# Optimization experiments

Hardware: AMD Instinct MI355X
Metric: run time of the kernel (lower is better)

Reference implementation:

```python
import jax, jax.numpy as jnp
import numpy as np

B, L, D, H = 4, 2048, 256, 8
FF = 128  # ff_intermediary_depth hard-coded in module
EPS = 1e-5


def layer_norm(x, g, b):
    mu = jnp.mean(x, axis=-1, keepdims=True)
    var = jnp.mean(jnp.square(x - mu), axis=-1, keepdims=True)
    return (x - mu) * jax.lax.rsqrt(var + EPS) * g + b


def setup_inputs() -> dict:
    key = jax.random.key(0)
    ks = jax.random.split(key, 8)
    s = 1.0 / np.sqrt(D)
    return {
        "seq": jax.random.normal(ks[0], (B, L, D), dtype=jnp.float32),
        "Wq": jax.random.normal(ks[1], (D, D * H), dtype=jnp.float32) * s,
        "Wk": jax.random.normal(ks[2], (D, D * H), dtype=jnp.float32) * s,
        "Wv": jax.random.normal(ks[3], (D, D * H), dtype=jnp.float32) * s,
        "Wo": jax.random.normal(ks[4], (D * H, D), dtype=jnp.float32) * (1.0 / np.sqrt(D * H)),
        "ln1_g": jnp.ones((D,), jnp.float32),
        "ln1_b": jnp.zeros((D,), jnp.float32),
        "W1": jax.random.normal(ks[5], (D, FF), dtype=jnp.float32) * s,
        "b1": jnp.zeros((FF,), jnp.float32),
        "W2": jax.random.normal(ks[6], (FF, D), dtype=jnp.float32) * (1.0 / np.sqrt(FF)),
        "b2": jnp.zeros((D,), jnp.float32),
        "ln2_g": jnp.ones((D,), jnp.float32),
        "ln2_b": jnp.zeros((D,), jnp.float32),
    }


def reference(seq, Wq, Wk, Wv, Wo, ln1_g, ln1_b, W1, b1, W2, b2, ln2_g, ln2_b):
    b, l, d = seq.shape
    # per-head dim equals full depth d (module quirk)
    q = (seq @ Wq).reshape(b, l, H, d)
    k = (seq @ Wk).reshape(b, l, H, d)
    v = (seq @ Wv).reshape(b, l, H, d)
    scores = jnp.einsum('bqhd,bkhd->bhqk', q, k) / jnp.sqrt(jnp.float32(d))
    a = jax.nn.softmax(scores, axis=-1)
    heads = jnp.einsum('bhqk,bkhd->bqhd', a, v).reshape(b, l, H * d)
    att_out = heads @ Wo
    x = layer_norm(seq + att_out, ln1_g, ln1_b)
    ff = jax.nn.relu(x @ W1 + b1) @ W2 + b2
    return layer_norm(x + ff, ln2_g, ln2_b)
```

## Files before the change

kernel.cpp:

```cpp
#include <hip/hip_runtime.h>


typedef unsigned short u16;
typedef unsigned int   u32;
typedef __bf16 bf16x8 __attribute__((ext_vector_type(8)));
typedef __bf16 bf16x2 __attribute__((ext_vector_type(2)));
typedef float  f32x4  __attribute__((ext_vector_type(4)));

#define MFMA(a, b, c) __builtin_amdgcn_mfma_f32_16x16x32_bf16(a, b, c, 0, 0, 0)

#if __has_builtin(__builtin_amdgcn_exp2f)
#define EXP2(x) __builtin_amdgcn_exp2f(x)
#else
#define EXP2(x) exp2f(x)
#endif

#if __has_builtin(__builtin_amdgcn_permlane16_swap) && \
    __has_builtin(__builtin_amdgcn_permlane32_swap)
#define HAS_PERMSWAP 1
#else
#define HAS_PERMSWAP 0
#endif

#define CEXP 0.09016844f

__device__ __forceinline__ float b2f(u16 h) {
  return __uint_as_float(((u32)h) << 16);
}
__device__ __forceinline__ u16 f2b(float f) {
  u32 u = __float_as_uint(f);
  u += 0x7FFFu + ((u >> 16) & 1u);
  return (u16)(u >> 16);
}
__device__ __forceinline__ u32 pkbf(float lo, float hi) {
  bf16x2 v;
  v[0] = (__bf16)lo;
  v[1] = (__bf16)hi;
  return __builtin_bit_cast(u32, v);
}
__device__ __forceinline__ bf16x8 ldb8(const u16* p) { return *(const bf16x8*)p; }

typedef const __attribute__((address_space(1))) u32* gas1_t;
typedef __attribute__((address_space(3))) u32* las3_t;
__device__ __forceinline__ void gload_lds16(const u16* g, u16* lds_base) {
  __builtin_amdgcn_global_load_lds((gas1_t)(const void*)g,
                                   (las3_t)(void*)lds_base, 16, 0, 0);
}

__device__ __forceinline__ int detect_f32(const void* seq) {
  const u32* s = (const u32*)seq;
  int cnt = 0;
  #pragma unroll
  for (int i = 0; i < 64; i++) {
    u32 e = (s[i] >> 7) & 0xFFu;
    cnt += (e >= 100u && e <= 140u) ? 1 : 0;
  }
  return cnt < 48;
}

__device__ __forceinline__ u16 ldw(const void* W, size_t idx, int isf32) {
  return isf32 ? f2b(((const float*)W)[idx]) : ((const u16*)W)[idx];
}

#if HAS_PERMSWAP
__device__ __forceinline__ bf16x8 softmax_pa(f32x4 sn0, f32x4 sn1,
                                             float& lsum) {
  float p00 = EXP2(sn0[0]), p01 = EXP2(sn0[1]);
  float p02 = EXP2(sn0[2]), p03 = EXP2(sn0[3]);
  float p10 = EXP2(sn1[0]), p11 = EXP2(sn1[1]);
  float p12 = EXP2(sn1[2]), p13 = EXP2(sn1[3]);
  lsum += ((p00 + p01) + (p02 + p03)) + ((p10 + p11) + (p12 + p13));
  u32 A0 = pkbf(p00, p01), A1 = pkbf(p02, p03);
  u32 B0 = pkbf(p10, p11), B1 = pkbf(p12, p13);
  auto ra = __builtin_amdgcn_permlane32_swap(A0, B0, false, false);
  auto rb = __builtin_amdgcn_permlane32_swap(A1, B1, false, false);
  auto sa = __builtin_amdgcn_permlane16_swap(ra[0], ra[1], false, false);
  auto sb = __builtin_amdgcn_permlane16_swap(rb[0], rb[1], false, false);
  uint4 wv;
  wv.x = sa[0];
  wv.y = sb[0];
  wv.z = sa[1];
  wv.w = sb[1];
  return __builtin_bit_cast(bf16x8, wv);
}
#endif

__device__ __forceinline__ void ingest_body(
    int bx, int tid, int isf32,
    const void* __restrict__ seq, const void* __restrict__ g1,
    const void* __restrict__ be1, const void* __restrict__ b1,
    const void* __restrict__ b2v, const void* __restrict__ g2,
    const void* __restrict__ be2, u16* __restrict__ sbuf,
    u16* __restrict__ vecs) {
  if (bx < 2048) {
    size_t i = (size_t)bx * 1024 + tid * 4;
    if (isf32) {
      const float* sp = (const float*)seq;
      u16 o0 = f2b(sp[i]), o1 = f2b(sp[i + 1]), o2 = f2b(sp[i + 2]), o3 = f2b(sp[i + 3]);
      uint2 ov; ov.x = (u32)o0 | ((u32)o1 << 16); ov.y = (u32)o2 | ((u32)o3 << 16);
      *(uint2*)(sbuf + i) = ov;
    } else {
      *(uint2*)(sbuf + i) = ((const uint2*)seq)[i >> 2];
    }
  } else {
    int t = bx - 2048;
    const void* src; int n;
    switch (t) {
      case 0: src = g1;  n = 256; break;
      case 1: src = be1; n = 256; break;
      case 2: src = b1;  n = 128; break;
      case 3: src = b2v; n = 256; break;
      case 4: src = g2;  n = 256; break;
      default: src = be2; n = 256; break;
    }
    if (tid < n) vecs[t * 256 + tid] = ldw(src, tid, isf32);
  }
}

__device__ __forceinline__ void pack_body(
    int px, int py, int tid, int isf32,
    const void* __restrict__ Wq, const void* __restrict__ Wk,
    const void* __restrict__ Wv, const void* __restrict__ Wo,
    const void* __restrict__ W1, const void* __restrict__ W2,
    u16* __restrict__ pWq, u16* __restrict__ pWk, u16* __restrict__ pWv,
    u16* __restrict__ pWo, u16* __restrict__ pW1, u16* __restrict__ pW2) {
  const void* W; u16* P; int K, N;
  switch (py) {
    case 0: W = Wq; P = pWq; K = 256;  N = 2048; break;
    case 1: W = Wk; P = pWk; K = 256;  N = 2048; break;
    case 2: W = Wv; P = pWv; K = 256;  N = 2048; break;
    case 3: W = Wo; P = pWo; K = 2048; N = 256;  break;
    case 4: W = W1; P = pW1; K = 256;  N = 128;  break;
    default: W = W2; P = pW2; K = 128; N = 256;  break;
  }
  int t = px * 256 + tid;
  int total = (K >> 5) * (N >> 4) * 64;
  if (t >= total) return;
  int lane = t & 63, f = t >> 6;
  int NT = N >> 4;
  int kt = f / NT, nt = f - kt * NT;
  int row0 = kt * 32 + ((lane >> 4) << 3);
  int col = nt * 16 + (lane & 15);
  u16 e[8];
  #pragma unroll
  for (int j = 0; j < 8; j++) e[j] = ldw(W, (size_t)(row0 + j) * N + col, isf32);
  uint4 u;
  u.x = (u32)e[0] | ((u32)e[1] << 16);
  u.y = (u32)e[2] | ((u32)e[3] << 16);
  u.z = (u32)e[4] | ((u32)e[5] << 16);
  u.w = (u32)e[6] | ((u32)e[7] << 16);
  *(uint4*)(P + ((size_t)f * 64 + lane) * 8) = u;
}

__global__ __launch_bounds__(256) void ingest_pack_kernel(
    const void* __restrict__ seq, const void* __restrict__ g1,
    const void* __restrict__ be1, const void* __restrict__ b1,
    const void* __restrict__ b2v, const void* __restrict__ g2,
    const void* __restrict__ be2, u16* __restrict__ sbuf,
    u16* __restrict__ vecs,
    const void* __restrict__ Wq, const void* __restrict__ Wk,
    const void* __restrict__ Wv, const void* __restrict__ Wo,
    const void* __restrict__ W1, const void* __restrict__ W2,
    u16* __restrict__ pWq, u16* __restrict__ pWk, u16* __restrict__ pWv,
    u16* __restrict__ pWo, u16* __restrict__ pW1, u16* __restrict__ pW2) {
  int isf32 = detect_f32(seq);
  int bx = blockIdx.x, tid = threadIdx.x;
  if (bx < 2054) {
    ingest_body(bx, tid, isf32, seq, g1, be1, b1, b2v, g2, be2, sbuf, vecs);
  } else {
    int bxp = bx - 2054;
    pack_body(bxp & 255, bxp >> 8, tid, isf32, Wq, Wk, Wv, Wo, W1, W2,
              pWq, pWk, pWv, pWo, pW1, pW2);
  }
}

__global__ __launch_bounds__(256, 2) void qkv_kernel(
    const u16* __restrict__ X,
    const u16* __restrict__ pWq, const u16* __restrict__ pWk,
    const u16* __restrict__ pWv,
    u16* __restrict__ Qo, u16* __restrict__ Ko, u16* __restrict__ Vo,
    int ntbase, int hc) {
  __shared__ u16 blds[64 * 512];
  const u16* Pw = (blockIdx.z == 0) ? pWq : ((blockIdx.z == 1) ? pWk : pWv);
  u16* Out = (blockIdx.z == 0) ? Qo : ((blockIdx.z == 1) ? Ko : Vo);
  int tid = threadIdx.x, lane = tid & 63, w = tid >> 6;
  int nt0 = ntbase + blockIdx.x * 8;
  int m0 = blockIdx.y * 128 + w * 32;
  bf16x8 af[2][8];
  #pragma unroll
  for (int kt = 0; kt < 8; kt++) {
    af[0][kt] = ldb8(X + (size_t)(m0 + (lane & 15)) * 256 + kt * 32 + (lane >> 4) * 8);
    af[1][kt] = ldb8(X + (size_t)(m0 + 16 + (lane & 15)) * 256 + kt * 32 + (lane >> 4) * 8);
  }
  #pragma unroll
  for (int i = 0; i < 16; i++) {
    int fl = w + i * 4;
    int kt = fl >> 3, nt = fl & 7;
    gload_lds16(Pw + ((size_t)(kt * 128 + nt0 + nt) * 64 + lane) * 8,
                blds + (size_t)fl * 512);
  }
  asm volatile("s_waitcnt vmcnt(0)" ::: "memory");
  __syncthreads();
  f32x4 acc[2][8] = {};
  #pragma unroll
  for (int kt = 0; kt < 8; kt++) {
    const u16* bp = blds + (size_t)kt * 8 * 512 + (size_t)lane * 8;
    #pragma unroll
    for (int nt = 0; nt < 8; nt++) {
      bf16x8 b = ldb8(bp + nt * 512);
      acc[0][nt] = MFMA(af[0][kt], b, acc[0][nt]);
      acc[1][nt] = MFMA(af[1][kt], b, acc[1][nt]);
    }
  }
  int isv = (blockIdx.z == 2);
  float sc = (blockIdx.z == 0) ? CEXP : 1.0f;
  int hl = blockIdx.x >> 1;
  int dd0 = (blockIdx.x & 1) * 128;
  int m0b = blockIdx.y * 128;
  int bi = m0b >> 11, l0 = m0b & 2047;
  __syncthreads();
  if (!isv) {
    #pragma unroll
    for (int mt = 0; mt < 2; mt++)
      #pragma unroll
      for (int nt = 0; nt < 8; nt++)
        #pragma unroll
        for (int r = 0; r < 4; r++)
          blds[(w * 32 + mt * 16 + (lane >> 4) * 4 + r) * 136 + nt * 16 + (lane & 15)] =
              f2b(acc[mt][nt][r] * sc);
    __syncthreads();
    #pragma unroll
    for (int i = 0; i < 8; i++) {
      int c = tid + i * 256;
      int mloc = c >> 4, q = c & 15;
      uint4 v = *(uint4*)(blds + mloc * 136 + q * 8);
      *(uint4*)(Out + ((size_t)(bi * hc + hl) * 2048 + l0 + mloc) * 256 + dd0 + q * 8) = v;
    }
  } else {
    #pragma unroll
    for (int mt = 0; mt < 2; mt++)
      #pragma unroll
      for (int nt = 0; nt < 8; nt++)
        #pragma unroll
        for (int r = 0; r < 4; r++)
          blds[(nt * 16 + (lane & 15)) * 136 + w * 32 + mt * 16 + (lane >> 4) * 4 + r] =
              f2b(acc[mt][nt][r]);
    __syncthreads();
    #pragma unroll
    for (int i = 0; i < 8; i++) {
      int c = tid + i * 256;
      int nloc = c >> 4, q = c & 15;
      uint4 v = *(uint4*)(blds + nloc * 136 + q * 8);
      *(uint4*)(Out + ((size_t)(bi * hc + hl) * 256 + dd0 + nloc) * 2048 + l0 + q * 8) = v;
    }
  }
}

__global__ __launch_bounds__(512, 4) void attn_kernel(
    const u16* __restrict__ Q, const u16* __restrict__ K,
    const u16* __restrict__ Vt, u16* __restrict__ O, int nbh) {
  __shared__ u16 kbuf[2 * 8192];
  __shared__ u16 vbuf[2 * 8192];
#if !HAS_PERMSWAP
  __shared__ u16 plds[8 * 640];
#endif
  int tid = threadIdx.x, lane = tid & 63, w = tid >> 6;
  int bi2 = blockIdx.x;
  int bh, qt;
  if (nbh >= 8) {
    int G = nbh >> 3;
    bh = (bi2 & 7) * G + (bi2 >> 3) % G;
    qt = bi2 / (8 * G);
  } else {
    bh = bi2 % nbh; qt = bi2 / nbh;
  }
  const u16* Qb  = Q  + (size_t)bh * 2048 * 256;
  const u16* Kb  = K  + (size_t)bh * 2048 * 256;
  const u16* Vtb = Vt + (size_t)bh * 256 * 2048;
  u16* Ob = O + (size_t)bh * 2048 * 256;
  int q0 = qt * 128 + w * 16;
  bf16x8 qf[8];
  #pragma unroll
  for (int kt = 0; kt < 8; kt++)
    qf[kt] = ldb8(Qb + (size_t)(q0 + (lane & 15)) * 256 + kt * 32 + (lane >> 4) * 8);
  f32x4 o[16] = {};
  float lsum = 0.f;
#if !HAS_PERMSWAP
  u16* pl = plds + (size_t)w * 640;
#endif

  #pragma unroll
  for (int j = 0; j < 2; j++) {
    int f = w * 2 + j;
    gload_lds16(Kb + (size_t)((f >> 3) * 16 + (lane & 15)) * 256 +
                    (f & 7) * 32 + (lane >> 4) * 8,
                kbuf + f * 512);
    gload_lds16(Vtb + (size_t)(f * 16 + (lane & 15)) * 2048 + (lane >> 4) * 8,
                vbuf + f * 512);
  }

  for (int t = 0; t < 64; t++) {
    int s0i = t * 32;
    asm volatile("s_waitcnt vmcnt(0)\ns_barrier" ::: "memory");
    if (t < 63) {
      int nb = (t + 1) & 1;
      #pragma unroll
      for (int j = 0; j < 2; j++) {
        int f = w * 2 + j;
        gload_lds16(Kb + (size_t)(s0i + 32 + (f >> 3) * 16 + (lane & 15)) * 256 +
                        (f & 7) * 32 + (lane >> 4) * 8,
                    kbuf + nb * 8192 + f * 512);
        gload_lds16(Vtb + (size_t)(f * 16 + (lane & 15)) * 2048 + s0i + 32 +
                        (lane >> 4) * 8,
                    vbuf + nb * 8192 + f * 512);
      }
    }
    const u16* kb = kbuf + (t & 1) * 8192;
    f32x4 s[2] = {};
    __builtin_amdgcn_s_setprio(1);
    #pragma unroll
    for (int ntk = 0; ntk < 2; ntk++)
      #pragma unroll
      for (int kt = 0; kt < 8; kt++) {
        bf16x8 a = ldb8(kb + (size_t)(ntk * 8 + kt) * 512 + lane * 8);
        s[ntk] = MFMA(a, qf[kt], s[ntk]);
      }
    __builtin_amdgcn_s_setprio(0);
#if HAS_PERMSWAP
    bf16x8 pa = softmax_pa(s[0], s[1], lsum);
#else
    #pragma unroll
    for (int ntk = 0; ntk < 2; ntk++) {
      float p0 = EXP2(s[ntk][0]);
      float p1 = EXP2(s[ntk][1]);
      float p2 = EXP2(s[ntk][2]);
      float p3 = EXP2(s[ntk][3]);
      lsum += (p0 + p1) + (p2 + p3);
      uint2 pk;
      pk.x = pkbf(p0, p1);
      pk.y = pkbf(p2, p3);
      *(uint2*)(pl + (lane & 15) * 40 + 16 * ntk + 4 * (lane >> 4)) = pk;
    }
    asm volatile("s_waitcnt lgkmcnt(0)" ::: "memory");
    bf16x8 pa = ldb8(pl + (lane & 15) * 40 + (lane >> 4) * 8);
    asm volatile("s_waitcnt lgkmcnt(0)" ::: "memory");
#endif
    const u16* vb0 = vbuf + (t & 1) * 8192;
    __builtin_amdgcn_s_setprio(1);
    #pragma unroll
    for (int nt = 0; nt < 16; nt++) {
      bf16x8 vb = ldb8(vb0 + (size_t)nt * 512 + lane * 8);
      o[nt] = MFMA(vb, pa, o[nt]);
    }
    __builtin_amdgcn_s_setprio(0);
  }
  float l = lsum;
  l += __shfl_xor(l, 16);
  l += __shfl_xor(l, 32);
  float linv = 1.0f / l;
  u16* el = kbuf + w * 1152;
  __syncthreads();
  #pragma unroll
  for (int g = 0; g < 4; g++) {
    if (g) asm volatile("s_waitcnt lgkmcnt(0)" ::: "memory");
    #pragma unroll
    for (int t2 = 0; t2 < 4; t2++) {
      int nt = g * 4 + t2;
      uint2 pk;
      pk.x = pkbf(o[nt][0] * linv, o[nt][1] * linv);
      pk.y = pkbf(o[nt][2] * linv, o[nt][3] * linv);
      *(uint2*)(el + (lane & 15) * 72 + t2 * 16 + 4 * (lane >> 4)) = pk;
    }
    asm volatile("s_waitcnt lgkmcnt(0)" ::: "memory");
    #pragma unroll
    for (int rep = 0; rep < 2; rep++) {
      int ch = lane + rep * 64;
      int row = ch >> 3, c8 = ch & 7;
      uint4 v = *(uint4*)(el + row * 72 + c8 * 8);
      *(uint4*)(Ob + (size_t)(q0 + row) * 256 + g * 64 + c8 * 8) = v;
    }
  }
}

__global__ __launch_bounds__(128) void accum_ln1_ffn_ln2_kernel(
    const u16* __restrict__ Oc, const u16* __restrict__ pWo,
    const u16* __restrict__ sbuf, const u16* __restrict__ vecs,
    const u16* __restrict__ pW1, const u16* __restrict__ pW2,
    const void* __restrict__ seq, void* __restrict__ out) {
  __shared__ u16 blds[2 * 32 * 512];
  int tid = threadIdx.x, lane = tid & 63, w = tid >> 6;
  int m0 = blockIdx.x * 32 + w * 16;
  int arow = m0 + (lane & 15);
  int bq = arow >> 11, lrow = arow & 2047;
  f32x4 acc[16] = {};
  #pragma unroll
  for (int i = 0; i < 16; i++) {
    int fl = w + i * 2;
    int ktg = fl >> 4, nt = fl & 15;
    gload_lds16(pWo + ((size_t)(ktg * 16 + nt) * 64 + lane) * 8,
                blds + (size_t)fl * 512);
  }
  asm volatile("s_waitcnt vmcnt(0)" ::: "memory");
  __syncthreads();
  for (int r = 0; r < 32; r++) {
    int k0 = r * 2;
    const u16* cur = blds + (size_t)(r & 1) * 16384;
    bf16x8 aA, aB;
    {
      int ktl = k0, hl = ktl >> 3;
      int d0 = (ktl & 7) * 32 + (lane >> 4) * 8;
      aA = ldb8(Oc + ((size_t)(bq * 8 + hl) * 2048 + lrow) * 256 + d0);
      ktl = k0 + 1; hl = ktl >> 3;
      d0 = (ktl & 7) * 32 + (lane >> 4) * 8;
      aB = ldb8(Oc + ((size_t)(bq * 8 + hl) * 2048 + lrow) * 256 + d0);
    }
    if (r < 31) {
      u16* nxt = blds + (size_t)((r + 1) & 1) * 16384;
      #pragma unroll
      for (int i = 0; i < 16; i++) {
        int fl = w + i * 2;
        int ktg = k0 + 2 + (fl >> 4), nt = fl & 15;
        gload_lds16(pWo + ((size_t)(ktg * 16 + nt) * 64 + lane) * 8,
                    nxt + (size_t)fl * 512);
      }
    }
    #pragma unroll
    for (int kl = 0; kl < 2; kl++) {
      bf16x8 a = kl ? aB : aA;
      const u16* bp = cur + (size_t)kl * 16 * 512 + (size_t)lane * 8;
      #pragma unroll
      for (int nt = 0; nt < 16; nt++) {
        bf16x8 b = ldb8(bp + nt * 512);
        acc[nt] = MFMA(a, b, acc[nt]);
      }
    }
    asm volatile("s_waitcnt vmcnt(0)" ::: "memory");
    __syncthreads();
  }
  int rbase = m0 + (lane >> 4) * 4;
  #pragma unroll
  for (int nt = 0; nt < 16; nt++) {
    int d = nt * 16 + (lane & 15);
    #pragma unroll
    for (int r = 0; r < 4; r++)
      acc[nt][r] += b2f(sbuf[(size_t)(rbase + r) * 256 + d]);
  }
  float mu[4], rs[4];
  #pragma unroll
  for (int r = 0; r < 4; r++) {
    float sm = 0.f;
    #pragma unroll
    for (int nt = 0; nt < 16; nt++) sm += acc[nt][r];
    sm += __shfl_xor(sm, 1); sm += __shfl_xor(sm, 2);
    sm += __shfl_xor(sm, 4); sm += __shfl_xor(sm, 8);
    mu[r] = sm * (1.0f / 256.0f);
    float v = 0.f;
    #pragma unroll
    for (int nt = 0; nt < 16; nt++) { float dd = acc[nt][r] - mu[r]; v += dd * dd; }
    v += __shfl_xor(v, 1); v += __shfl_xor(v, 2);
    v += __shfl_xor(v, 4); v += __shfl_xor(v, 8);
    rs[r] = rsqrtf(v * (1.0f / 256.0f) + 1e-5f);
  }
  u16* xw = blds + (size_t)w * 16 * 264;
  uint2 xp[16];
  #pragma unroll
  for (int nt = 0; nt < 16; nt++) {
    int d = nt * 16 + (lane & 15);
    float gg = b2f(vecs[d]), bb = b2f(vecs[256 + d]);
    u16 e[4];
    #pragma unroll
    for (int r = 0; r < 4; r++) {
      e[r] = f2b((acc[nt][r] - mu[r]) * rs[r] * gg + bb);
      xw[((lane >> 4) * 4 + r) * 264 + d] = e[r];
    }
    xp[nt].x = (u32)e[0] | ((u32)e[1] << 16);
    xp[nt].y = (u32)e[2] | ((u32)e[3] << 16);
  }
  __syncthreads();
  int isf32 = detect_f32(seq);
  u16* hb = blds + 16384 + (size_t)w * 16 * 136;
  f32x4 acc1[8] = {};
  #pragma unroll
  for (int kt = 0; kt < 8; kt++) {
    bf16x8 a = ldb8(xw + (size_t)(lane & 15) * 264 + kt * 32 + (lane >> 4) * 8);
    const u16* bp = pW1 + ((size_t)kt * 8 * 64 + lane) * 8;
    #pragma unroll
    for (int nt = 0; nt < 8; nt++) {
      bf16x8 b = ldb8(bp + nt * 512);
      acc1[nt] = MFMA(a, b, acc1[nt]);
    }
  }
  #pragma unroll
  for (int nt = 0; nt < 8; nt++) {
    int col = nt * 16 + (lane & 15);
    float bb = b2f(vecs[512 + col]);
    #pragma unroll
    for (int r = 0; r < 4; r++) {
      float h = fmaxf(acc1[nt][r] + bb, 0.f);
      hb[((lane >> 4) * 4 + r) * 136 + col] = f2b(h);
    }
  }
  __syncthreads();
  f32x4 acc2[16] = {};
  #pragma unroll
  for (int ks = 0; ks < 4; ks++) {
    bf16x8 a = ldb8(hb + (size_t)(lane & 15) * 136 + ks * 32 + (lane >> 4) * 8);
    const u16* bp = pW2 + ((size_t)ks * 16 * 64 + lane) * 8;
    #pragma unroll
    for (int nt = 0; nt < 16; nt++) {
      bf16x8 b = ldb8(bp + nt * 512);
      acc2[nt] = MFMA(a, b, acc2[nt]);
    }
  }
  #pragma unroll
  for (int nt = 0; nt < 16; nt++) {
    int d = nt * 16 + (lane & 15);
    float bb = b2f(vecs[768 + d]);
    acc2[nt][0] += bb + b2f((u16)(xp[nt].x & 0xFFFF));
    acc2[nt][1] += bb + b2f((u16)(xp[nt].x >> 16));
    acc2[nt][2] += bb + b2f((u16)(xp[nt].y & 0xFFFF));
    acc2[nt][3] += bb + b2f((u16)(xp[nt].y >> 16));
  }
  float mu2[4], rs2[4];
  #pragma unroll
  for (int r = 0; r < 4; r++) {
    float sm = 0.f;
    #pragma unroll
    for (int nt = 0; nt < 16; nt++) sm += acc2[nt][r];
    sm += __shfl_xor(sm, 1); sm += __shfl_xor(sm, 2);
    sm += __shfl_xor(sm, 4); sm += __shfl_xor(sm, 8);
    mu2[r] = sm * (1.0f / 256.0f);
    float v = 0.f;
    #pragma unroll
    for (int nt = 0; nt < 16; nt++) { float dd = acc2[nt][r] - mu2[r]; v += dd * dd; }
    v += __shfl_xor(v, 1); v += __shfl_xor(v, 2);
    v += __shfl_xor(v, 4); v += __shfl_xor(v, 8);
    rs2[r] = rsqrtf(v * (1.0f / 256.0f) + 1e-5f);
  }
  #pragma unroll
  for (int nt = 0; nt < 16; nt++) {
    int d = nt * 16 + (lane & 15);
    float gg = b2f(vecs[1024 + d]), bb = b2f(vecs[1280 + d]);
    #pragma unroll
    for (int r = 0; r < 4; r++) {
      float val = (acc2[nt][r] - mu2[r]) * rs2[r] * gg + bb;
      size_t idx = (size_t)(rbase + r) * 256 + d;
      if (isf32) ((float*)out)[idx] = val;
      else       ((u16*)out)[idx]   = f2b(val);
    }
  }
}

__global__ __launch_bounds__(256) void accum_kernel(
    const u16* __restrict__ Oc, const u16* __restrict__ pWo,
    float* __restrict__ att_out, int kt0, int hc) {
  __shared__ u16 blds[64 * 512];
  int tid = threadIdx.x, lane = tid & 63, w = tid >> 6;
  int m0 = blockIdx.x * 64 + w * 16;
  int arow = m0 + (lane & 15);
  int bq = arow >> 11, lrow = arow & 2047;
  int ktn = hc * 8;
  f32x4 acc[16] = {};
  for (int k0 = 0; k0 < ktn; k0 += 4) {
    __syncthreads();
    #pragma unroll
    for (int i = 0; i < 16; i++) {
      int fl = w + i * 4;
      int ktg = kt0 + k0 + (fl >> 4), nt = fl & 15;
      gload_lds16(pWo + ((size_t)(ktg * 16 + nt) * 64 + lane) * 8,
                  blds + (size_t)fl * 512);
    }
    asm volatile("s_waitcnt vmcnt(0)" ::: "memory");
    __syncthreads();
    #pragma unroll
    for (int kl = 0; kl < 4; kl++) {
      int ktl = k0 + kl;
      int hl = ktl >> 3;
      int d0 = (ktl & 7) * 32 + (lane >> 4) * 8;
      bf16x8 a = ldb8(Oc + ((size_t)(bq * hc + hl) * 2048 + lrow) * 256 + d0);
      const u16* bp = blds + (size_t)kl * 16 * 512 + (size_t)lane * 8;
      #pragma unroll
      for (int nt = 0; nt < 16; nt++) {
        bf16x8 b = ldb8(bp + nt * 512);
        acc[nt] = MFMA(a, b, acc[nt]);
      }
    }
  }
  int rbase = m0 + (lane >> 4) * 4;
  #pragma unroll
  for (int nt = 0; nt < 16; nt++) {
    int d = nt * 16 + (lane & 15);
    #pragma unroll
    for (int r = 0; r < 4; r++)
      att_out[(size_t)(rbase + r) * 256 + d] += acc[nt][r];
  }
}

__global__ __launch_bounds__(256) void ln1_kernel(
    const float* __restrict__ att_out, const u16* __restrict__ sbuf,
    const u16* __restrict__ vecs, u16* __restrict__ xout) {
  int tid = threadIdx.x, lane = tid & 63, w = tid >> 6;
  int row = blockIdx.x * 4 + w;
  const float* ar = att_out + (size_t)row * 256;
  f32x4 a = *(const f32x4*)(ar + lane * 4);
  uint2 sv = *(const uint2*)(sbuf + (size_t)row * 256 + lane * 4);
  float y[4];
  y[0] = a[0] + b2f((u16)(sv.x & 0xFFFF));
  y[1] = a[1] + b2f((u16)(sv.x >> 16));
  y[2] = a[2] + b2f((u16)(sv.y & 0xFFFF));
  y[3] = a[3] + b2f((u16)(sv.y >> 16));
  float sm = y[0] + y[1] + y[2] + y[3];
  sm += __shfl_xor(sm, 1);  sm += __shfl_xor(sm, 2);  sm += __shfl_xor(sm, 4);
  sm += __shfl_xor(sm, 8);  sm += __shfl_xor(sm, 16); sm += __shfl_xor(sm, 32);
  float mu = sm * (1.0f / 256.0f);
  float v = 0.f;
  #pragma unroll
  for (int j = 0; j < 4; j++) { float d = y[j] - mu; v += d * d; }
  v += __shfl_xor(v, 1);  v += __shfl_xor(v, 2);  v += __shfl_xor(v, 4);
  v += __shfl_xor(v, 8);  v += __shfl_xor(v, 16); v += __shfl_xor(v, 32);
  float rs = rsqrtf(v * (1.0f / 256.0f) + 1e-5f);
  u16 o[4];
  #pragma unroll
  for (int j = 0; j < 4; j++) {
    int d = lane * 4 + j;
    o[j] = f2b((y[j] - mu) * rs * b2f(vecs[d]) + b2f(vecs[256 + d]));
  }
  uint2 ov; ov.x = (u32)o[0] | ((u32)o[1] << 16); ov.y = (u32)o[2] | ((u32)o[3] << 16);
  *(uint2*)(xout + (size_t)row * 256 + lane * 4) = ov;
}

__global__ __launch_bounds__(128) void ffn_ln2_kernel(
    const u16* __restrict__ x, const u16* __restrict__ pW1,
    const u16* __restrict__ pW2, const u16* __restrict__ vecs,
    const void* __restrict__ seq, void* __restrict__ out) {
  __shared__ u16 hbuf[2 * 16 * 136];
  int isf32 = detect_f32(seq);
  int tid = threadIdx.x, lane = tid & 63, w = tid >> 6;
  int m0 = blockIdx.x * 32 + w * 16;
  int arow = m0 + (lane & 15);
  u16* hb = hbuf + w * 16 * 136;
  f32x4 acc1[8] = {};
  #pragma unroll
  for (int kt = 0; kt < 8; kt++) {
    bf16x8 a = ldb8(x + (size_t)arow * 256 + kt * 32 + (lane >> 4) * 8);
    const u16* bp = pW1 + ((size_t)kt * 8 * 64 + lane) * 8;
    #pragma unroll
    for (int nt = 0; nt < 8; nt++) {
      bf16x8 b = ldb8(bp + nt * 512);
      acc1[nt] = MFMA(a, b, acc1[nt]);
    }
  }
  #pragma unroll
  for (int nt = 0; nt < 8; nt++) {
    int col = nt * 16 + (lane & 15);
    float bb = b2f(vecs[512 + col]);
    #pragma unroll
    for (int r = 0; r < 4; r++) {
      float h = fmaxf(acc1[nt][r] + bb, 0.f);
      hb[((lane >> 4) * 4 + r) * 136 + col] = f2b(h);
    }
  }
  __syncthreads();
  f32x4 acc2[16] = {};
  #pragma unroll
  for (int ks = 0; ks < 4; ks++) {
    bf16x8 a = ldb8(hb + (lane & 15) * 136 + ks * 32 + (lane >> 4) * 8);
    const u16* bp = pW2 + ((size_t)ks * 16 * 64 + lane) * 8;
    #pragma unroll
    for (int nt = 0; nt < 16; nt++) {
      bf16x8 b = ldb8(bp + nt * 512);
      acc2[nt] = MFMA(a, b, acc2[nt]);
    }
  }
  int rbase = m0 + (lane >> 4) * 4;
  #pragma unroll
  for (int nt = 0; nt < 16; nt++) {
    int d = nt * 16 + (lane & 15);
    float bb = b2f(vecs[768 + d]);
    #pragma unroll
    for (int r = 0; r < 4; r++)
      acc2[nt][r] += bb + b2f(x[(size_t)(rbase + r) * 256 + d]);
  }
  float mu[4], rs[4];
  #pragma unroll
  for (int r = 0; r < 4; r++) {
    float sm = 0.f;
    #pragma unroll
    for (int nt = 0; nt < 16; nt++) sm += acc2[nt][r];
    sm += __shfl_xor(sm, 1); sm += __shfl_xor(sm, 2);
    sm += __shfl_xor(sm, 4); sm += __shfl_xor(sm, 8);
    mu[r] = sm * (1.0f / 256.0f);
    float v = 0.f;
    #pragma unroll
    for (int nt = 0; nt < 16; nt++) { float dd = acc2[nt][r] - mu[r]; v += dd * dd; }
    v += __shfl_xor(v, 1); v += __shfl_xor(v, 2);
    v += __shfl_xor(v, 4); v += __shfl_xor(v, 8);
    rs[r] = rsqrtf(v * (1.0f / 256.0f) + 1e-5f);
  }
  #pragma unroll
  for (int nt = 0; nt < 16; nt++) {
    int d = nt * 16 + (lane & 15);
    float gg = b2f(vecs[1024 + d]), bb = b2f(vecs[1280 + d]);
    #pragma unroll
    for (int r = 0; r < 4; r++) {
      float val = (acc2[nt][r] - mu[r]) * rs[r] * gg + bb;
      size_t idx = (size_t)(rbase + r) * 256 + d;
      if (isf32) ((float*)out)[idx] = val;
      else       ((u16*)out)[idx]   = f2b(val);
    }
  }
}

__global__ __launch_bounds__(256) void sentinel_kernel(void* out, int n,
                                                       const void* seq) {
  int isf32 = detect_f32(seq);
  int i = blockIdx.x * 256 + threadIdx.x;
  if (i < n) {
    if (isf32) ((float*)out)[i] = 777.0f;
    else       ((u16*)out)[i]   = 0x4442;
  }
}

extern "C" void kernel_launch(void* const* d_in, const int* in_sizes, int n_in,
                              void* d_out, int out_size, void* d_ws, size_t ws_size,
                              hipStream_t stream) {
  (void)in_sizes; (void)n_in;
  const void* seq  = d_in[0];
  const void* Wq   = d_in[1];
  const void* Wk   = d_in[2];
  const void* Wv   = d_in[3];
  const void* Wo   = d_in[4];
  const void* g1   = d_in[5];
  const void* be1  = d_in[6];
  const void* W1   = d_in[7];
  const void* b1   = d_in[8];
  const void* W2   = d_in[9];
  const void* b2   = d_in[10];
  const void* g2   = d_in[11];
  const void* be2  = d_in[12];

  size_t o = 0;
  u16* ws = (u16*)d_ws;
  u16* pWq = ws + o; o += 524288;
  u16* pWk = ws + o; o += 524288;
  u16* pWv = ws + o; o += 524288;
  u16* pWo = ws + o; o += 524288;
  u16* pW1 = ws + o; o += 32768;
  u16* pW2 = ws + o; o += 32768;
  float* att = (float*)(ws + o); o += 4194304;
  u16* xb   = ws + o; o += 2097152;
  u16* sbuf = ws + o; o += 2097152;
  u16* vecs = ws + o; o += 2048;
  size_t fixed_elems = o;

  int hc = 0;
  for (int c = 8; c >= 1; c >>= 1) {
    size_t need = (fixed_elems + (size_t)4 * c * 2097152) * 2;
    if (need <= ws_size) { hc = c; break; }
  }
  if (hc == 0) {
    sentinel_kernel<<<dim3((out_size + 255) / 256), 256, 0, stream>>>(
        d_out, out_size, seq);
    return;
  }
  u16* Qc = ws + o; o += (size_t)hc * 2097152;
  u16* Kc = ws + o; o += (size_t)hc * 2097152;
  u16* Vc = ws + o; o += (size_t)hc * 2097152;
  u16* Oc = ws + o;

  ingest_pack_kernel<<<dim3(2054 + 1536), 256, 0, stream>>>(
      seq, g1, be1, b1, b2, g2, be2, sbuf, vecs,
      Wq, Wk, Wv, Wo, W1, W2, pWq, pWk, pWv, pWo, pW1, pW2);
  if (hc == 8) {
    qkv_kernel<<<dim3(16, 64, 3), 256, 0, stream>>>(
        sbuf, pWq, pWk, pWv, Qc, Kc, Vc, 0, 8);
    attn_kernel<<<dim3(32 * 16), 512, 0, stream>>>(Qc, Kc, Vc, Oc, 32);
    accum_ln1_ffn_ln2_kernel<<<dim3(256), 128, 0, stream>>>(
        Oc, pWo, sbuf, vecs, pW1, pW2, seq, (void*)d_out);
  } else {
    hipMemsetAsync(att, 0, 2097152 * sizeof(float), stream);
    int nchunks = 8 / hc;
    for (int c = 0; c < nchunks; c++) {
      int nbh = 4 * hc;
      qkv_kernel<<<dim3(2 * hc, 64, 3), 256, 0, stream>>>(
          sbuf, pWq, pWk, pWv, Qc, Kc, Vc, c * hc * 16, hc);
      attn_kernel<<<dim3(nbh * 16), 512, 0, stream>>>(Qc, Kc, Vc, Oc, nbh);
      accum_kernel<<<dim3(128), 256, 0, stream>>>(Oc, pWo, att, c * hc * 8, hc);
    }
    ln1_kernel<<<dim3(2048), 256, 0, stream>>>(att, sbuf, vecs, xb);
    ffn_ln2_kernel<<<dim3(256), 128, 0, stream>>>(xb, pW1, pW2, vecs, seq,
                                                  (void*)d_out);
  }
}
```

Baseline: 341.8 us.

## Reuse staged QKV weight tile across four row blocks per workgroup

Each qkv workgroup now handles 512 rows instead of 128, looping four times over the same weight tile held in LDS, so weight loads into LDS are cut by a factor of four. The activation fragments for the next row block are prefetched while the current one is being computed. The epilogue now stages through a small per-wave LDS buffer instead of the block-wide buffer, which removes block-level barriers. The grid shrinks fourfold (768 blocks), which may reduce occupancy and latency hiding, and the extra LDS buffer raises LDS use per block.

```diff
diff --git a/kernel.cpp b/kernel.cpp
--- a/kernel.cpp
+++ b/kernel.cpp
@@ -181,17 +181,16 @@
     u16* __restrict__ Qo, u16* __restrict__ Ko, u16* __restrict__ Vo,
     int ntbase, int hc) {
   __shared__ u16 blds[64 * 512];
+  __shared__ u16 ebuf[4 * 1280];
   const u16* Pw = (blockIdx.z == 0) ? pWq : ((blockIdx.z == 1) ? pWk : pWv);
   u16* Out = (blockIdx.z == 0) ? Qo : ((blockIdx.z == 1) ? Ko : Vo);
   int tid = threadIdx.x, lane = tid & 63, w = tid >> 6;
   int nt0 = ntbase + blockIdx.x * 8;
-  int m0 = blockIdx.y * 128 + w * 32;
-  bf16x8 af[2][8];
-  #pragma unroll
-  for (int kt = 0; kt < 8; kt++) {
-    af[0][kt] = ldb8(X + (size_t)(m0 + (lane & 15)) * 256 + kt * 32 + (lane >> 4) * 8);
-    af[1][kt] = ldb8(X + (size_t)(m0 + 16 + (lane & 15)) * 256 + kt * 32 + (lane >> 4) * 8);
-  }
+  int isv = (blockIdx.z == 2);
+  float sc = (blockIdx.z == 0) ? CEXP : 1.0f;
+  int hl = blockIdx.x >> 1;
+  int dd0 = (blockIdx.x & 1) * 128;
+  u16* eb = ebuf + (size_t)w * 1280;
   #pragma unroll
   for (int i = 0; i < 16; i++) {
     int fl = w + i * 4;
@@ -199,59 +198,87 @@
     gload_lds16(Pw + ((size_t)(kt * 128 + nt0 + nt) * 64 + lane) * 8,
                 blds + (size_t)fl * 512);
   }
+  bf16x8 af[2][8];
+  {
+    int m0 = blockIdx.y * 512 + w * 32;
+    #pragma unroll
+    for (int kt = 0; kt < 8; kt++) {
+      af[0][kt] = ldb8(X + (size_t)(m0 + (lane & 15)) * 256 + kt * 32 + (lane >> 4) * 8);
+      af[1][kt] = ldb8(X + (size_t)(m0 + 16 + (lane & 15)) * 256 + kt * 32 + (lane >> 4) * 8);
+    }
+  }
   asm volatile("s_waitcnt vmcnt(0)" ::: "memory");
   __syncthreads();
-  f32x4 acc[2][8] = {};
-  #pragma unroll
-  for (int kt = 0; kt < 8; kt++) {
-    const u16* bp = blds + (size_t)kt * 8 * 512 + (size_t)lane * 8;
-    #pragma unroll
-    for (int nt = 0; nt < 8; nt++) {
-      bf16x8 b = ldb8(bp + nt * 512);
-      acc[0][nt] = MFMA(af[0][kt], b, acc[0][nt]);
-      acc[1][nt] = MFMA(af[1][kt], b, acc[1][nt]);
-    }
-  }
-  int isv = (blockIdx.z == 2);
-  float sc = (blockIdx.z == 0) ? CEXP : 1.0f;
-  int hl = blockIdx.x >> 1;
-  int dd0 = (blockIdx.x & 1) * 128;
-  int m0b = blockIdx.y * 128;
-  int bi = m0b >> 11, l0 = m0b & 2047;
-  __syncthreads();
-  if (!isv) {
-    #pragma unroll
-    for (int mt = 0; mt < 2; mt++)
+  for (int y = 0; y < 4; y++) {
+    int m0b = blockIdx.y * 512 + y * 128;
+    f32x4 acc[2][8] = {};
+    #pragma unroll
+    for (int kt = 0; kt < 8; kt++) {
+      const u16* bp = blds + (size_t)kt * 8 * 512 + (size_t)lane * 8;
       #pragma unroll
-      for (int nt = 0; nt < 8; nt++)
+      for (int nt = 0; nt < 8; nt++) {
+        bf16x8 b = ldb8(bp + nt * 512);
+        acc[0][nt] = MFMA(af[0][kt], b, acc[0][nt]);
+        acc[1][nt] = MFMA(af[1][kt], b, acc[1][nt]);
+      }
+    }
+    if (y < 3) {
+      int m1 = m0b + 128 + w * 32;
+      #pragma unroll
+      for (int kt = 0; kt < 8; kt++) {
+        af[0][kt] = ldb8(X + (size_t)(m1 + (lane & 15)) * 256 + kt * 32 + (lane >> 4) * 8);
+        af[1][kt] = ldb8(X + (size_t)(m1 + 16 + (lane & 15)) * 256 + kt * 32 + (lane >> 4) * 8);
+      }
+    }
+    int bi = m0b >> 11, l0 = m0b & 2047;
+    if (!isv) {
+      #pragma unroll
+      for (int g = 0; g < 4; g++) {
         #pragma unroll
-        for (int r = 0; r < 4; r++)
-          blds[(w * 32 + mt * 16 + (lane >> 4) * 4 + r) * 136 + nt * 16 + (lane & 15)] =
-              f2b(acc[mt][nt][r] * sc);
-    __syncthreads();
-    #pragma unroll
-    for (int i = 0; i < 8; i++) {
-      int c = tid + i * 256;
-      int mloc = c >> 4, q = c & 15;
-      uint4 v = *(uint4*)(blds + mloc * 136 + q * 8);
-      *(uint4*)(Out + ((size_t)(bi * hc + hl) * 2048 + l0 + mloc) * 256 + dd0 + q * 8) = v;
-    }
-  } else {
-    #pragma unroll
-    for (int mt = 0; mt < 2; mt++)
+        for (int mt = 0; mt < 2; mt++)
+          #pragma unroll
+          for (int nt2 = 0; nt2 < 2; nt2++) {
+            int nt = g * 2 + nt2;
+            #pragma unroll
+            for (int r = 0; r < 4; r++)
+              eb[(mt * 16 + (lane >> 4) * 4 + r) * 40 + nt2 * 16 + (lane & 15)] =
+                  f2b(acc[mt][nt][r] * sc);
+          }
+        asm volatile("s_waitcnt lgkmcnt(0)" ::: "memory");
+        #pragma unroll
+        for (int rep = 0; rep < 2; rep++) {
+          int ch = lane + rep * 64;
+          int row = ch >> 2, c8 = ch & 3;
+          uint4 v = *(uint4*)(eb + row * 40 + c8 * 8);
+          *(uint4*)(Out + ((size_t)(bi * hc + hl) * 2048 + l0 + w * 32 + row) * 256 +
+                    dd0 + g * 32 + c8 * 8) = v;
+        }
+        asm volatile("s_waitcnt lgkmcnt(0)" ::: "memory");
+      }
+    } else {
       #pragma unroll
-      for (int nt = 0; nt < 8; nt++)
+      for (int g = 0; g < 4; g++) {
         #pragma unroll
-        for (int r = 0; r < 4; r++)
-          blds[(nt * 16 + (lane & 15)) * 136 + w * 32 + mt * 16 + (lane >> 4) * 4 + r] =
-              f2b(acc[mt][nt][r]);
-    __syncthreads();
-    #pragma unroll
-    for (int i = 0; i < 8; i++) {
-      int c = tid + i * 256;
-      int nloc = c >> 4, q = c & 15;
-      uint4 v = *(uint4*)(blds + nloc * 136 + q * 8);
-      *(uint4*)(Out + ((size_t)(bi * hc + hl) * 256 + dd0 + nloc) * 2048 + l0 + q * 8) = v;
+        for (int mt = 0; mt < 2; mt++)
+          #pragma unroll
+          for (int nt2 = 0; nt2 < 2; nt2++) {
+            int nt = g * 2 + nt2;
+            #pragma unroll
+            for (int r = 0; r < 4; r++)
+              eb[(nt2 * 16 + (lane & 15)) * 40 + mt * 16 + (lane >> 4) * 4 + r] =
+                  f2b(acc[mt][nt][r]);
+          }
+        asm volatile("s_waitcnt lgkmcnt(0)" ::: "memory");
+        #pragma unroll
+        for (int rep = 0; rep < 2; rep++) {
+          int ch = lane + rep * 64;
+          int dc = ch >> 2, c8 = ch & 3;
+          uint4 v = *(uint4*)(eb + dc * 40 + c8 * 8);
+          *(uint4*)(Out + ((size_t)(bi * hc + hl) * 256 + dd0 + g * 32 + dc) * 2048 +
+                    l0 + w * 32 + c8 * 8) = v;
+        }
+        asm volatile("s_waitcnt lgkmcnt(0)" ::: "memory");
+      }
     }
   }
 }
@@ -772,7 +799,7 @@
       seq, g1, be1, b1, b2, g2, be2, sbuf, vecs,
       Wq, Wk, Wv, Wo, W1, W2, pWq, pWk, pWv, pWo, pW1, pW2);
   if (hc == 8) {
-    qkv_kernel<<<dim3(16, 64, 3), 256, 0, stream>>>(
+    qkv_kernel<<<dim3(16, 16, 3), 256, 0, stream>>>(
         sbuf, pWq, pWk, pWv, Qc, Kc, Vc, 0, 8);
     attn_kernel<<<dim3(32 * 16), 512, 0, stream>>>(Qc, Kc, Vc, Oc, 32);
     accum_ln1_ffn_ln2_kernel<<<dim3(256), 128, 0, stream>>>(
@@ -782,7 +809,7 @@
     int nchunks = 8 / hc;
     for (int c = 0; c < nchunks; c++) {
       int nbh = 4 * hc;
-      qkv_kernel<<<dim3(2 * hc, 64, 3), 256, 0, stream>>>(
+      qkv_kernel<<<dim3(2 * hc, 16, 3), 256, 0, stream>>>(
           sbuf, pWq, pWk, pWv, Qc, Kc, Vc, c * hc * 16, hc);
       attn_kernel<<<dim3(nbh * 16), 512, 0, stream>>>(Qc, Kc, Vc, Oc, nbh);
       accum_kernel<<<dim3(128), 256, 0, stream>>>(Oc, pWo, att, c * hc * 8, hc);
```

After: 333.8 us, median of 2. -2.4%, faster.
